# Kernel tuning notes

Hardware: AMD Instinct MI355X
Metric: run time of the kernel (lower is better)

## Reference

```python
import jax, jax.numpy as jnp
import numpy as np

N_NODES = 50000
N_EDGES = 800000
IN_CH = 128
HIDDEN = [128, 128]
OUT_CH = 64


def _glorot(key, shape):
    fan_in, fan_out = shape
    lim = (6.0 / (fan_in + fan_out)) ** 0.5
    return jax.random.uniform(key, shape, jnp.float32, -lim, lim)


def setup_inputs() -> dict:
    key = jax.random.key(0)
    ks = jax.random.split(key, 12)
    x = jax.random.normal(ks[0], (N_NODES, IN_CH), jnp.float32)
    edge_index = jax.random.randint(ks[1], (2, N_EDGES), 0, N_NODES, jnp.int64)
    dims = [IN_CH] + HIDDEN + [OUT_CH]
    params = {}
    for i in range(len(dims) - 1):
        d_in, d_out = dims[i], dims[i + 1]
        params[f"W_l{i}"] = _glorot(ks[2 + 3 * i], (d_in, d_out))      # neighbor weight
        params[f"W_r{i}"] = _glorot(ks[3 + 3 * i], (d_in, d_out))      # root/self weight
        params[f"b{i}"] = jnp.zeros((d_out,), jnp.float32)
    return {"x": x, "edge_index": edge_index, **params}


def _sage_conv(x, src, dst, W_l, W_r, b):
    # mean-aggregate neighbor features: messages flow src -> dst
    n = x.shape[0]
    agg = jax.ops.segment_sum(x[src], dst, num_segments=n)            # [N, d_in]
    cnt = jax.ops.segment_sum(jnp.ones((src.shape[0],), x.dtype), dst, num_segments=n)
    mean = agg / jnp.maximum(cnt, 1.0)[:, None]
    # PyG SAGEConv: lin_l(mean_neighbors) + lin_r(x_self); bias on lin_l only
    return mean @ W_l + x @ W_r + b


def reference(x, edge_index,
              W_l0, W_r0, b0,
              W_l1, W_r1, b1,
              W_l2, W_r2, b2):
    src, dst = edge_index[0], edge_index[1]
    h = _sage_conv(x, src, dst, W_l0, W_r0, b0)
    h = jax.nn.elu(h)
    h = _sage_conv(h, src, dst, W_l1, W_r1, b1)
    h = jax.nn.elu(h)
    out = _sage_conv(h, src, dst, W_l2, W_r2, b2)
    return out
```

## Files before the change

### kernel.cpp

```cpp
#include <hip/hip_runtime.h>
#include <math.h>

#define N_NODES 50000
#define N_EDGES 800000
#define IN_CH 128
#define NBUCK 196
#define BCAP 5120
#define EPB 4082

typedef unsigned short ushort_t;
typedef unsigned int uint_t;
typedef __attribute__((ext_vector_type(8))) short bf16x8;
typedef __attribute__((ext_vector_type(4))) float f32x4;

static __device__ __forceinline__ ushort_t f32_to_bf16(float f) {
    uint_t u = __float_as_uint(f);
    uint_t r = (u + 0x7fffu + ((u >> 16) & 1u)) >> 16;
    return (ushort_t)r;
}

static __device__ __forceinline__ void acc8(float* a, uint4 v) {
    a[0] += __uint_as_float(v.x << 16); a[1] += __uint_as_float(v.x & 0xffff0000u);
    a[2] += __uint_as_float(v.y << 16); a[3] += __uint_as_float(v.y & 0xffff0000u);
    a[4] += __uint_as_float(v.z << 16); a[5] += __uint_as_float(v.z & 0xffff0000u);
    a[6] += __uint_as_float(v.w << 16); a[7] += __uint_as_float(v.w & 0xffff0000u);
}

__global__ __launch_bounds__(256) void binA(
    const int* __restrict__ src, const int* __restrict__ dst,
    uint_t* __restrict__ gbcnt, uint_t* __restrict__ gbuck) {
    __shared__ uint_t hist[NBUCK];
    __shared__ uint_t excl_s[NBUCK];
    __shared__ uint_t gbase[NBUCK];
    __shared__ uint_t cur[NBUCK];
    __shared__ uint_t pfx[256];
    __shared__ uint_t stage[4096];
    __shared__ uint_t gpos[4096];
    const int t = threadIdx.x;
    const int e0 = blockIdx.x * EPB;
    const int e1 = min(e0 + EPB, N_EDGES);

    for (int i = t; i < NBUCK; i += 256) hist[i] = 0;
    __syncthreads();
    for (int e = e0 + t; e < e1; e += 256) atomicAdd(&hist[dst[e] >> 8], 1u);
    __syncthreads();
    uint_t own = (t < NBUCK) ? hist[t] : 0;
    pfx[t] = own;
    __syncthreads();
    for (int d = 1; d < 256; d <<= 1) {
        uint_t v = (t >= d) ? pfx[t - d] : 0;
        __syncthreads();
        pfx[t] += v;
        __syncthreads();
    }
    if (t < NBUCK) {
        uint_t excl = pfx[t] - own;
        excl_s[t] = excl;
        cur[t] = excl;
        gbase[t] = atomicAdd(&gbcnt[t], own);
    }
    __syncthreads();
    for (int e = e0 + t; e < e1; e += 256) {
        int d_ = dst[e];
        int b = d_ >> 8;
        uint_t p = atomicAdd(&cur[b], 1u);
        stage[p] = ((uint_t)(d_ & 255) << 16) | (uint_t)src[e];
        gpos[p] = (uint_t)b * BCAP + gbase[b] + (p - excl_s[b]);
    }
    __syncthreads();
    const int n = e1 - e0;
    for (int i = t; i < n; i += 256) gbuck[gpos[i]] = stage[i];
}

__global__ __launch_bounds__(256) void binB(
    const uint_t* __restrict__ gbcnt, const uint_t* __restrict__ gbuck,
    int* __restrict__ offs, int* __restrict__ ebuf) {
    __shared__ uint_t pairs[BCAP];
    __shared__ int stage[BCAP];
    __shared__ uint_t bscan[256];
    __shared__ uint_t h[256];
    __shared__ uint_t psc[256];
    __shared__ int cur[256];
    const int b = blockIdx.x;
    const int t = threadIdx.x;

    uint_t g = (t < NBUCK) ? gbcnt[t] : 0;
    bscan[t] = g;
    __syncthreads();
    for (int d = 1; d < 256; d <<= 1) {
        uint_t v = (t >= d) ? bscan[t - d] : 0;
        __syncthreads();
        bscan[t] += v;
        __syncthreads();
    }
    const int base = (b > 0) ? (int)bscan[b - 1] : 0;
    const uint_t n = gbcnt[b];

    for (uint_t i = t; i < n; i += 256) pairs[i] = gbuck[(size_t)b * BCAP + i];
    h[t] = 0;
    __syncthreads();
    for (uint_t i = t; i < n; i += 256) atomicAdd(&h[(pairs[i] >> 16) & 255u], 1u);
    __syncthreads();
    uint_t own = h[t];
    psc[t] = own;
    __syncthreads();
    for (int d = 1; d < 256; d <<= 1) {
        uint_t v = (t >= d) ? psc[t - d] : 0;
        __syncthreads();
        psc[t] += v;
        __syncthreads();
    }
    const int excl = (int)(psc[t] - own);
    const int node = b * 256 + t;
    if (node <= N_NODES) offs[node] = base + excl;
    cur[t] = excl;
    __syncthreads();
    for (uint_t i = t; i < n; i += 256) {
        uint_t p = pairs[i];
        int l = (p >> 16) & 255;
        int pos = atomicAdd(&cur[l], 1);
        stage[pos] = (int)(p & 0xFFFFu);
    }
    __syncthreads();
    for (uint_t i = t; i < n; i += 256) ebuf[base + (int)i] = stage[i];
}

__global__ __launch_bounds__(256) void cvt_x(const float* __restrict__ x,
                                             ushort_t* __restrict__ xb,
                                             uint_t* __restrict__ gbcnt, int n8) {
    int i = blockIdx.x * 256 + threadIdx.x;
    if (blockIdx.x == 0 && threadIdx.x < NBUCK) gbcnt[threadIdx.x] = 0;
    if (i >= n8) return;
    const float* p = x + (size_t)i * 8;
    float4 lo = *(const float4*)p;
    float4 hi = *(const float4*)(p + 4);
    bf16x8 r;
    r[0] = (short)f32_to_bf16(lo.x); r[1] = (short)f32_to_bf16(lo.y);
    r[2] = (short)f32_to_bf16(lo.z); r[3] = (short)f32_to_bf16(lo.w);
    r[4] = (short)f32_to_bf16(hi.x); r[5] = (short)f32_to_bf16(hi.y);
    r[6] = (short)f32_to_bf16(hi.z); r[7] = (short)f32_to_bf16(hi.w);
    *(bf16x8*)&xb[(size_t)i * 8] = r;
}

__global__ __launch_bounds__(256) void prep_all(
    const float* __restrict__ Wl0, const float* __restrict__ Wr0,
    const float* __restrict__ Wl1, const float* __restrict__ Wr1,
    const float* __restrict__ Wl2, const float* __restrict__ Wr2,
    ushort_t* __restrict__ Bt0, ushort_t* __restrict__ Bt1,
    ushort_t* __restrict__ Bt2) {
    int i = blockIdx.x * 256 + threadIdx.x;
    const float* Wl;
    const float* Wr;
    ushort_t* Bt;
    int C;
    if (i < 32768) {
        Wl = Wl0; Wr = Wr0; Bt = Bt0; C = 128;
    } else if (i < 65536) {
        i -= 32768; Wl = Wl1; Wr = Wr1; Bt = Bt1; C = 128;
    } else if (i < 81920) {
        i -= 65536; Wl = Wl2; Wr = Wr2; Bt = Bt2; C = 64;
    } else {
        return;
    }
    int c = i / 256, k = i % 256;
    float v = (k < 128) ? Wl[(size_t)k * C + c] : Wr[(size_t)(k - 128) * C + c];
    Bt[i] = f32_to_bf16(v);
}

__global__ __launch_bounds__(256) void gather_mean(
    const int* __restrict__ offs, const int* __restrict__ ebuf,
    const ushort_t* __restrict__ feat, ushort_t* __restrict__ M, int nNodes) {
    const int wl = threadIdx.x >> 6;
    const int lane = threadIdx.x & 63;
    const int q = lane >> 4;
    const int cl = (lane & 15) * 8;
    const int nw = gridDim.x * 4;

    for (int wid = blockIdx.x * 4 + wl; wid < nNodes; wid += nw) {
        const int o0 = offs[wid], o1 = offs[wid + 1];
        const float inv = 1.0f / fmaxf((float)(o1 - o0), 1.0f);
        float a0[8] = {0.f, 0.f, 0.f, 0.f, 0.f, 0.f, 0.f, 0.f};
        float a1[8] = {0.f, 0.f, 0.f, 0.f, 0.f, 0.f, 0.f, 0.f};
        int j = o0;
        for (; j + 8 <= o1; j += 8) {
            int s0 = ebuf[j + q];
            int s1 = ebuf[j + 4 + q];
            uint4 v0 = *(const uint4*)&feat[(size_t)s0 * 128 + cl];
            uint4 v1 = *(const uint4*)&feat[(size_t)s1 * 128 + cl];
            acc8(a0, v0);
            acc8(a1, v1);
        }
        if (j + 4 <= o1) {
            int s0 = ebuf[j + q];
            uint4 v0 = *(const uint4*)&feat[(size_t)s0 * 128 + cl];
            acc8(a0, v0);
            j += 4;
        }
        if (j + q < o1) {
            int s1 = ebuf[j + q];
            uint4 v1 = *(const uint4*)&feat[(size_t)s1 * 128 + cl];
            acc8(a1, v1);
        }
#pragma unroll
        for (int k = 0; k < 8; ++k) a0[k] += a1[k];
#pragma unroll
        for (int k = 0; k < 8; ++k) {
            a0[k] += __shfl_xor(a0[k], 16);
            a0[k] += __shfl_xor(a0[k], 32);
        }
        if (lane < 16) {
            uint4 o;
            o.x = (uint_t)f32_to_bf16(a0[0] * inv) | ((uint_t)f32_to_bf16(a0[1] * inv) << 16);
            o.y = (uint_t)f32_to_bf16(a0[2] * inv) | ((uint_t)f32_to_bf16(a0[3] * inv) << 16);
            o.z = (uint_t)f32_to_bf16(a0[4] * inv) | ((uint_t)f32_to_bf16(a0[5] * inv) << 16);
            o.w = (uint_t)f32_to_bf16(a0[6] * inv) | ((uint_t)f32_to_bf16(a0[7] * inv) << 16);
            *(uint4*)&M[(size_t)wid * 128 + cl] = o;
        }
    }
}

template <int C, bool ELU, bool OUT_F32>
__global__ __launch_bounds__(256) void gemm_fused(
    const ushort_t* __restrict__ M, const ushort_t* __restrict__ X,
    const ushort_t* __restrict__ Bt, const float* __restrict__ bias,
    void* __restrict__ out_v, int nNodes) {
    const int tid = threadIdx.x;
    const int wave = tid >> 6, lane = tid & 63;
    const int lrow = lane & 15, lgrp = lane >> 4;
    const int rowbase = blockIdx.x * 64 + (wave >> 1) * 32;
    const int colbase = blockIdx.y * 64 + (wave & 1) * 32;

    f32x4 acc[2][2] = {};

#pragma unroll
    for (int half = 0; half < 2; ++half) {
        const ushort_t* A = half ? X : M;
#pragma unroll
        for (int ks = 0; ks < 4; ++ks) {
            const int k0 = ks * 32 + lgrp * 8;
            bf16x8 a[2], bf[2];
#pragma unroll
            for (int mi = 0; mi < 2; ++mi) {
                int r = rowbase + mi * 16 + lrow;
                r = min(r, nNodes - 1);
                a[mi] = *(const bf16x8*)&A[(size_t)r * 128 + k0];
            }
#pragma unroll
            for (int ni = 0; ni < 2; ++ni) {
                int c = colbase + ni * 16 + lrow;
                bf[ni] = *(const bf16x8*)&Bt[(size_t)c * 256 + half * 128 + k0];
            }
#pragma unroll
            for (int mi = 0; mi < 2; ++mi)
#pragma unroll
                for (int ni = 0; ni < 2; ++ni)
                    acc[mi][ni] = __builtin_amdgcn_mfma_f32_16x16x32_bf16(
                        a[mi], bf[ni], acc[mi][ni], 0, 0, 0);
        }
    }

#pragma unroll
    for (int ni = 0; ni < 2; ++ni) {
        const int c = colbase + ni * 16 + lrow;
        const float bv = bias[c];
#pragma unroll
        for (int mi = 0; mi < 2; ++mi) {
#pragma unroll
            for (int j = 0; j < 4; ++j) {
                int r = rowbase + mi * 16 + lgrp * 4 + j;
                if (r >= nNodes) continue;
                float v = acc[mi][ni][j] + bv;
                if (ELU) v = v > 0.f ? v : expm1f(v);
                if (OUT_F32) ((float*)out_v)[(size_t)r * C + c] = v;
                else ((ushort_t*)out_v)[(size_t)r * C + c] = f32_to_bf16(v);
            }
        }
    }
}

extern "C" void kernel_launch(void* const* d_in, const int* in_sizes, int n_in,
                              void* d_out, int out_size, void* d_ws, size_t ws_size,
                              hipStream_t stream) {
    const float* x = (const float*)d_in[0];
    const int* ei = (const int*)d_in[1];
    const int* src = ei;
    const int* dst = ei + N_EDGES;
    const float* Wl0 = (const float*)d_in[2];
    const float* Wr0 = (const float*)d_in[3];
    const float* b0 = (const float*)d_in[4];
    const float* Wl1 = (const float*)d_in[5];
    const float* Wr1 = (const float*)d_in[6];
    const float* b1 = (const float*)d_in[7];
    const float* Wl2 = (const float*)d_in[8];
    const float* Wr2 = (const float*)d_in[9];
    const float* b2 = (const float*)d_in[10];
    float* out = (float*)d_out;

    int* wsi = (int*)d_ws;
    int* offs = wsi;
    uint_t* gbcnt = (uint_t*)(offs + 51200);
    int* ebuf = (int*)(gbcnt + 256);
    uint_t* gbuck = (uint_t*)(ebuf + 800000);
    ushort_t* Bt0 = (ushort_t*)(gbuck + NBUCK * BCAP);
    ushort_t* Bt1 = Bt0 + 128 * 256;
    ushort_t* Bt2 = Bt1 + 128 * 256;
    const long long NB = (long long)N_NODES * 128;
    ushort_t* xb = Bt2 + 64 * 256;
    ushort_t* Mb = xb + NB;
    ushort_t* hA = Mb + NB;
    ushort_t* hB = hA + NB;

    cvt_x<<<(N_NODES * 16 + 255) / 256, 256, 0, stream>>>(x, xb, gbcnt, N_NODES * 16);
    prep_all<<<(81920 + 255) / 256, 256, 0, stream>>>(
        Wl0, Wr0, Wl1, Wr1, Wl2, Wr2, Bt0, Bt1, Bt2);

    binA<<<NBUCK, 256, 0, stream>>>(src, dst, gbcnt, gbuck);
    binB<<<NBUCK, 256, 0, stream>>>(gbcnt, gbuck, offs, ebuf);

    const int GATHER_GRID = 2048;
    const int GR = (N_NODES + 63) / 64;

    gather_mean<<<GATHER_GRID, 256, 0, stream>>>(offs, ebuf, xb, Mb, N_NODES);
    gemm_fused<128, true, false><<<dim3(GR, 2), 256, 0, stream>>>(
        Mb, xb, Bt0, b0, hA, N_NODES);

    gather_mean<<<GATHER_GRID, 256, 0, stream>>>(offs, ebuf, hA, Mb, N_NODES);
    gemm_fused<128, true, false><<<dim3(GR, 2), 256, 0, stream>>>(
        Mb, hA, Bt1, b1, hB, N_NODES);

    gather_mean<<<GATHER_GRID, 256, 0, stream>>>(offs, ebuf, hB, Mb, N_NODES);
    gemm_fused<64, false, true><<<dim3(GR, 1), 256, 0, stream>>>(
        Mb, hB, Bt2, b2, out, N_NODES);
}
```

Baseline: 209.8 us.

## Merge prep kernels, unroll gather to 16 edges, cover all columns per GEMM block

Fuses edge binning, weight transpose and x conversion into one launch, and clears the bucket counters with a memset in place of the conversion kernel. Widens the gather loop to four independent accumulators so more row loads are in flight per wave. The GEMM now has each block compute all output columns, so the A tiles are loaded once instead of once per column half. Trade-offs: the fused prep kernel holds the binning kernel's large shared-memory footprint for every block, which may lower occupancy of the conversion blocks, and the GEMM uses more registers.

```diff
diff --git a/kernel.cpp b/kernel.cpp
--- a/kernel.cpp
+++ b/kernel.cpp
@@ -8,6 +8,10 @@
 #define BCAP 5120
 #define EPB 4082
 
+#define NB_BINA 196
+#define NB_PREP 320
+#define NB_CVT 3125
+
 typedef unsigned short ushort_t;
 typedef unsigned int uint_t;
 typedef __attribute__((ext_vector_type(8))) short bf16x8;
@@ -26,9 +30,15 @@
     a[6] += __uint_as_float(v.w << 16); a[7] += __uint_as_float(v.w & 0xffff0000u);
 }
 
-__global__ __launch_bounds__(256) void binA(
+__global__ __launch_bounds__(256) void mega_prep(
     const int* __restrict__ src, const int* __restrict__ dst,
-    uint_t* __restrict__ gbcnt, uint_t* __restrict__ gbuck) {
+    uint_t* __restrict__ gbcnt, uint_t* __restrict__ gbuck,
+    const float* __restrict__ Wl0, const float* __restrict__ Wr0,
+    const float* __restrict__ Wl1, const float* __restrict__ Wr1,
+    const float* __restrict__ Wl2, const float* __restrict__ Wr2,
+    ushort_t* __restrict__ Bt0, ushort_t* __restrict__ Bt1,
+    ushort_t* __restrict__ Bt2,
+    const float* __restrict__ x, ushort_t* __restrict__ xb) {
     __shared__ uint_t hist[NBUCK];
     __shared__ uint_t excl_s[NBUCK];
     __shared__ uint_t gbase[NBUCK];
@@ -36,40 +46,74 @@
     __shared__ uint_t pfx[256];
     __shared__ uint_t stage[4096];
     __shared__ uint_t gpos[4096];
+
+    const int bid = blockIdx.x;
     const int t = threadIdx.x;
-    const int e0 = blockIdx.x * EPB;
-    const int e1 = min(e0 + EPB, N_EDGES);
-
-    for (int i = t; i < NBUCK; i += 256) hist[i] = 0;
-    __syncthreads();
-    for (int e = e0 + t; e < e1; e += 256) atomicAdd(&hist[dst[e] >> 8], 1u);
-    __syncthreads();
-    uint_t own = (t < NBUCK) ? hist[t] : 0;
-    pfx[t] = own;
-    __syncthreads();
-    for (int d = 1; d < 256; d <<= 1) {
-        uint_t v = (t >= d) ? pfx[t - d] : 0;
-        __syncthreads();
-        pfx[t] += v;
-        __syncthreads();
-    }
-    if (t < NBUCK) {
-        uint_t excl = pfx[t] - own;
-        excl_s[t] = excl;
-        cur[t] = excl;
-        gbase[t] = atomicAdd(&gbcnt[t], own);
-    }
-    __syncthreads();
-    for (int e = e0 + t; e < e1; e += 256) {
-        int d_ = dst[e];
-        int b = d_ >> 8;
-        uint_t p = atomicAdd(&cur[b], 1u);
-        stage[p] = ((uint_t)(d_ & 255) << 16) | (uint_t)src[e];
-        gpos[p] = (uint_t)b * BCAP + gbase[b] + (p - excl_s[b]);
-    }
-    __syncthreads();
-    const int n = e1 - e0;
-    for (int i = t; i < n; i += 256) gbuck[gpos[i]] = stage[i];
+
+    if (bid < NB_BINA) {
+        const int e0 = bid * EPB;
+        const int e1 = min(e0 + EPB, N_EDGES);
+        for (int i = t; i < NBUCK; i += 256) hist[i] = 0;
+        __syncthreads();
+        for (int e = e0 + t; e < e1; e += 256) atomicAdd(&hist[dst[e] >> 8], 1u);
+        __syncthreads();
+        uint_t own = (t < NBUCK) ? hist[t] : 0;
+        pfx[t] = own;
+        __syncthreads();
+        for (int d = 1; d < 256; d <<= 1) {
+            uint_t v = (t >= d) ? pfx[t - d] : 0;
+            __syncthreads();
+            pfx[t] += v;
+            __syncthreads();
+        }
+        if (t < NBUCK) {
+            uint_t excl = pfx[t] - own;
+            excl_s[t] = excl;
+            cur[t] = excl;
+            gbase[t] = atomicAdd(&gbcnt[t], own);
+        }
+        __syncthreads();
+        for (int e = e0 + t; e < e1; e += 256) {
+            int d_ = dst[e];
+            int b = d_ >> 8;
+            uint_t p = atomicAdd(&cur[b], 1u);
+            stage[p] = ((uint_t)(d_ & 255) << 16) | (uint_t)src[e];
+            gpos[p] = (uint_t)b * BCAP + gbase[b] + (p - excl_s[b]);
+        }
+        __syncthreads();
+        const int n = e1 - e0;
+        for (int i = t; i < n; i += 256) gbuck[gpos[i]] = stage[i];
+    } else if (bid < NB_BINA + NB_PREP) {
+        int i = (bid - NB_BINA) * 256 + t;
+        const float* Wl;
+        const float* Wr;
+        ushort_t* Bt;
+        int C;
+        if (i < 32768) {
+            Wl = Wl0; Wr = Wr0; Bt = Bt0; C = 128;
+        } else if (i < 65536) {
+            i -= 32768; Wl = Wl1; Wr = Wr1; Bt = Bt1; C = 128;
+        } else if (i < 81920) {
+            i -= 65536; Wl = Wl2; Wr = Wr2; Bt = Bt2; C = 64;
+        } else {
+            return;
+        }
+        int c = i / 256, k = i % 256;
+        float v = (k < 128) ? Wl[(size_t)k * C + c] : Wr[(size_t)(k - 128) * C + c];
+        Bt[i] = f32_to_bf16(v);
+    } else {
+        int i = (bid - NB_BINA - NB_PREP) * 256 + t;
+        if (i >= NB_CVT * 256) return;
+        const float* p = x + (size_t)i * 8;
+        float4 lo = *(const float4*)p;
+        float4 hi = *(const float4*)(p + 4);
+        bf16x8 r;
+        r[0] = (short)f32_to_bf16(lo.x); r[1] = (short)f32_to_bf16(lo.y);
+        r[2] = (short)f32_to_bf16(lo.z); r[3] = (short)f32_to_bf16(lo.w);
+        r[4] = (short)f32_to_bf16(hi.x); r[5] = (short)f32_to_bf16(hi.y);
+        r[6] = (short)f32_to_bf16(hi.z); r[7] = (short)f32_to_bf16(hi.w);
+        *(bf16x8*)&xb[(size_t)i * 8] = r;
+    }
 }
 
 __global__ __launch_bounds__(256) void binB(
@@ -125,48 +169,6 @@
     for (uint_t i = t; i < n; i += 256) ebuf[base + (int)i] = stage[i];
 }
 
-__global__ __launch_bounds__(256) void cvt_x(const float* __restrict__ x,
-                                             ushort_t* __restrict__ xb,
-                                             uint_t* __restrict__ gbcnt, int n8) {
-    int i = blockIdx.x * 256 + threadIdx.x;
-    if (blockIdx.x == 0 && threadIdx.x < NBUCK) gbcnt[threadIdx.x] = 0;
-    if (i >= n8) return;
-    const float* p = x + (size_t)i * 8;
-    float4 lo = *(const float4*)p;
-    float4 hi = *(const float4*)(p + 4);
-    bf16x8 r;
-    r[0] = (short)f32_to_bf16(lo.x); r[1] = (short)f32_to_bf16(lo.y);
-    r[2] = (short)f32_to_bf16(lo.z); r[3] = (short)f32_to_bf16(lo.w);
-    r[4] = (short)f32_to_bf16(hi.x); r[5] = (short)f32_to_bf16(hi.y);
-    r[6] = (short)f32_to_bf16(hi.z); r[7] = (short)f32_to_bf16(hi.w);
-    *(bf16x8*)&xb[(size_t)i * 8] = r;
-}
-
-__global__ __launch_bounds__(256) void prep_all(
-    const float* __restrict__ Wl0, const float* __restrict__ Wr0,
-    const float* __restrict__ Wl1, const float* __restrict__ Wr1,
-    const float* __restrict__ Wl2, const float* __restrict__ Wr2,
-    ushort_t* __restrict__ Bt0, ushort_t* __restrict__ Bt1,
-    ushort_t* __restrict__ Bt2) {
-    int i = blockIdx.x * 256 + threadIdx.x;
-    const float* Wl;
-    const float* Wr;
-    ushort_t* Bt;
-    int C;
-    if (i < 32768) {
-        Wl = Wl0; Wr = Wr0; Bt = Bt0; C = 128;
-    } else if (i < 65536) {
-        i -= 32768; Wl = Wl1; Wr = Wr1; Bt = Bt1; C = 128;
-    } else if (i < 81920) {
-        i -= 65536; Wl = Wl2; Wr = Wr2; Bt = Bt2; C = 64;
-    } else {
-        return;
-    }
-    int c = i / 256, k = i % 256;
-    float v = (k < 128) ? Wl[(size_t)k * C + c] : Wr[(size_t)(k - 128) * C + c];
-    Bt[i] = f32_to_bf16(v);
-}
-
 __global__ __launch_bounds__(256) void gather_mean(
     const int* __restrict__ offs, const int* __restrict__ ebuf,
     const ushort_t* __restrict__ feat, ushort_t* __restrict__ M, int nNodes) {
@@ -181,28 +183,40 @@
         const float inv = 1.0f / fmaxf((float)(o1 - o0), 1.0f);
         float a0[8] = {0.f, 0.f, 0.f, 0.f, 0.f, 0.f, 0.f, 0.f};
         float a1[8] = {0.f, 0.f, 0.f, 0.f, 0.f, 0.f, 0.f, 0.f};
+        float a2[8] = {0.f, 0.f, 0.f, 0.f, 0.f, 0.f, 0.f, 0.f};
+        float a3[8] = {0.f, 0.f, 0.f, 0.f, 0.f, 0.f, 0.f, 0.f};
         int j = o0;
+        for (; j + 16 <= o1; j += 16) {
+            int s0 = ebuf[j + q];
+            int s1 = ebuf[j + 4 + q];
+            int s2 = ebuf[j + 8 + q];
+            int s3 = ebuf[j + 12 + q];
+            uint4 v0 = *(const uint4*)&feat[(size_t)s0 * 128 + cl];
+            uint4 v1 = *(const uint4*)&feat[(size_t)s1 * 128 + cl];
+            uint4 v2 = *(const uint4*)&feat[(size_t)s2 * 128 + cl];
+            uint4 v3 = *(const uint4*)&feat[(size_t)s3 * 128 + cl];
+            acc8(a0, v0); acc8(a1, v1); acc8(a2, v2); acc8(a3, v3);
+        }
         for (; j + 8 <= o1; j += 8) {
             int s0 = ebuf[j + q];
             int s1 = ebuf[j + 4 + q];
             uint4 v0 = *(const uint4*)&feat[(size_t)s0 * 128 + cl];
             uint4 v1 = *(const uint4*)&feat[(size_t)s1 * 128 + cl];
-            acc8(a0, v0);
-            acc8(a1, v1);
+            acc8(a0, v0); acc8(a1, v1);
         }
         if (j + 4 <= o1) {
-            int s0 = ebuf[j + q];
-            uint4 v0 = *(const uint4*)&feat[(size_t)s0 * 128 + cl];
-            acc8(a0, v0);
+            int s2 = ebuf[j + q];
+            uint4 v2 = *(const uint4*)&feat[(size_t)s2 * 128 + cl];
+            acc8(a2, v2);
             j += 4;
         }
         if (j + q < o1) {
-            int s1 = ebuf[j + q];
-            uint4 v1 = *(const uint4*)&feat[(size_t)s1 * 128 + cl];
-            acc8(a1, v1);
-        }
-#pragma unroll
-        for (int k = 0; k < 8; ++k) a0[k] += a1[k];
+            int s3 = ebuf[j + q];
+            uint4 v3 = *(const uint4*)&feat[(size_t)s3 * 128 + cl];
+            acc8(a3, v3);
+        }
+#pragma unroll
+        for (int k = 0; k < 8; ++k) a0[k] += a1[k] + (a2[k] + a3[k]);
 #pragma unroll
         for (int k = 0; k < 8; ++k) {
             a0[k] += __shfl_xor(a0[k], 16);
@@ -224,13 +238,14 @@
     const ushort_t* __restrict__ M, const ushort_t* __restrict__ X,
     const ushort_t* __restrict__ Bt, const float* __restrict__ bias,
     void* __restrict__ out_v, int nNodes) {
+    constexpr int NI = C / 32;
     const int tid = threadIdx.x;
     const int wave = tid >> 6, lane = tid & 63;
     const int lrow = lane & 15, lgrp = lane >> 4;
     const int rowbase = blockIdx.x * 64 + (wave >> 1) * 32;
-    const int colbase = blockIdx.y * 64 + (wave & 1) * 32;
-
-    f32x4 acc[2][2] = {};
+    const int colbase = (wave & 1) * (C / 2);
+
+    f32x4 acc[2][NI] = {};
 
 #pragma unroll
     for (int half = 0; half < 2; ++half) {
@@ -238,7 +253,7 @@
 #pragma unroll
         for (int ks = 0; ks < 4; ++ks) {
             const int k0 = ks * 32 + lgrp * 8;
-            bf16x8 a[2], bf[2];
+            bf16x8 a[2], bf[NI];
 #pragma unroll
             for (int mi = 0; mi < 2; ++mi) {
                 int r = rowbase + mi * 16 + lrow;
@@ -246,21 +261,21 @@
                 a[mi] = *(const bf16x8*)&A[(size_t)r * 128 + k0];
             }
 #pragma unroll
-            for (int ni = 0; ni < 2; ++ni) {
+            for (int ni = 0; ni < NI; ++ni) {
                 int c = colbase + ni * 16 + lrow;
                 bf[ni] = *(const bf16x8*)&Bt[(size_t)c * 256 + half * 128 + k0];
             }
 #pragma unroll
             for (int mi = 0; mi < 2; ++mi)
 #pragma unroll
-                for (int ni = 0; ni < 2; ++ni)
+                for (int ni = 0; ni < NI; ++ni)
                     acc[mi][ni] = __builtin_amdgcn_mfma_f32_16x16x32_bf16(
                         a[mi], bf[ni], acc[mi][ni], 0, 0, 0);
         }
     }
 
 #pragma unroll
-    for (int ni = 0; ni < 2; ++ni) {
+    for (int ni = 0; ni < NI; ++ni) {
         const int c = colbase + ni * 16 + lrow;
         const float bv = bias[c];
 #pragma unroll
@@ -310,25 +325,24 @@
     ushort_t* hA = Mb + NB;
     ushort_t* hB = hA + NB;
 
-    cvt_x<<<(N_NODES * 16 + 255) / 256, 256, 0, stream>>>(x, xb, gbcnt, N_NODES * 16);
-    prep_all<<<(81920 + 255) / 256, 256, 0, stream>>>(
-        Wl0, Wr0, Wl1, Wr1, Wl2, Wr2, Bt0, Bt1, Bt2);
-
-    binA<<<NBUCK, 256, 0, stream>>>(src, dst, gbcnt, gbuck);
+    hipMemsetAsync(gbcnt, 0, NBUCK * sizeof(uint_t), stream);
+    mega_prep<<<NB_BINA + NB_PREP + NB_CVT, 256, 0, stream>>>(
+        src, dst, gbcnt, gbuck,
+        Wl0, Wr0, Wl1, Wr1, Wl2, Wr2, Bt0, Bt1, Bt2, x, xb);
     binB<<<NBUCK, 256, 0, stream>>>(gbcnt, gbuck, offs, ebuf);
 
     const int GATHER_GRID = 2048;
     const int GR = (N_NODES + 63) / 64;
 
     gather_mean<<<GATHER_GRID, 256, 0, stream>>>(offs, ebuf, xb, Mb, N_NODES);
-    gemm_fused<128, true, false><<<dim3(GR, 2), 256, 0, stream>>>(
+    gemm_fused<128, true, false><<<GR, 256, 0, stream>>>(
         Mb, xb, Bt0, b0, hA, N_NODES);
 
     gather_mean<<<GATHER_GRID, 256, 0, stream>>>(offs, ebuf, hA, Mb, N_NODES);
-    gemm_fused<128, true, false><<<dim3(GR, 2), 256, 0, stream>>>(
+    gemm_fused<128, true, false><<<GR, 256, 0, stream>>>(
         Mb, hA, Bt1, b1, hB, N_NODES);
 
     gather_mean<<<GATHER_GRID, 256, 0, stream>>>(offs, ebuf, hB, Mb, N_NODES);
-    gemm_fused<64, false, true><<<dim3(GR, 1), 256, 0, stream>>>(
+    gemm_fused<64, false, true><<<GR, 256, 0, stream>>>(
         Mb, hB, Bt2, b2, out, N_NODES);
 }
```

Result: slower. 228.4 us (+8.9%).
